# Kernel tuning notes

Measured on AMD Instinct MI355X. Metric: run time of the kernel, lower is better.

The kernel has to match this reference:

```python
import jax, jax.numpy as jnp
import numpy as np

IN_C = 256
OUT_C = 256
K = 3
PAD = 1
SCALE = 1.0 / np.sqrt(IN_C * K * K)  # 1/sqrt(in_channels * k^2)
EPS = 1e-8
NEG_SLOPE = 0.2


def setup_inputs() -> dict:
    key = jax.random.key(0)
    k0, k1, k2, k3 = jax.random.split(key, 4)
    B, H, W, SD = 8, 128, 128, 512
    x = jax.random.normal(k0, (B, IN_C, H, W), dtype=jnp.float32)
    style = jax.random.normal(k1, (B, SD), dtype=jnp.float32)
    weight = jax.random.normal(k2, (OUT_C, IN_C, K, K), dtype=jnp.float32)
    mod_w = jax.random.normal(k3, (IN_C, SD), dtype=jnp.float32) / np.sqrt(SD)
    mod_b = jnp.zeros((IN_C,), dtype=jnp.float32)
    return {"x": x, "style": style, "weight": weight, "mod_w": mod_w, "mod_b": mod_b}


def reference(x, style, weight, mod_w, mod_b):
    # modulation: Linear(style_dim -> in_channels)
    s = style @ mod_w.T + mod_b                      # [B, I]
    # per-sample modulated weight [B, O, I, k, k]
    w = SCALE * weight[None] * s[:, None, :, None, None]
    # demodulation over (I, kh, kw)
    demod = jax.lax.rsqrt(jnp.sum(w * w, axis=(2, 3, 4)) + EPS)  # [B, O]
    w = w * demod[:, :, None, None, None]
    # per-sample conv (equivalent to groups=batch trick), vmapped over batch
    def conv_one(xi, wi):  # xi: [I,H,W], wi: [O,I,k,k]
        return jax.lax.conv_general_dilated(
            xi[None], wi, window_strides=(1, 1),
            padding=((PAD, PAD), (PAD, PAD)),
            dimension_numbers=("NCHW", "OIHW", "NCHW"))[0]
    y = jax.vmap(conv_one)(x, w)                     # [B, O, H, W]
    # LeakyReLU(0.2)
    return jnp.where(y >= 0, y, NEG_SLOPE * y)
```

## Files before the change

### kernel.cpp

```cpp
#include <hip/hip_runtime.h>
#include <hip/hip_bf16.h>
#include <cstddef>
#include <cstdint>


#define IN_C 256
#define OUT_C 256
#define HW 16384
#define W_IMG 128
#define SDIM 512
#define SCALE_F 0.020833333333333332f
#define EPS_F 1e-8f
#define NEG_SLOPE 0.2f

#define XROWB 8320
#define WTILEB 8192

typedef short bf16x8 __attribute__((ext_vector_type(8)));
typedef float f32x4 __attribute__((ext_vector_type(4)));

__device__ __forceinline__ unsigned short f2bf(float f) {
  unsigned u = __builtin_bit_cast(unsigned, f);
  unsigned r = u + 0x7FFFu + ((u >> 16) & 1u);
  return (unsigned short)(r >> 16);
}

__device__ __forceinline__ void glds16(const void* g, void* l) {
  __builtin_amdgcn_global_load_lds(
      (const __attribute__((address_space(1))) unsigned int*)g,
      (__attribute__((address_space(3))) unsigned int*)l, 16, 0, 0);
}

__global__ void style_mod_kernel(const float* __restrict__ style,
                                 const float* __restrict__ mod_w,
                                 const float* __restrict__ mod_b,
                                 float* __restrict__ s_out) {
  const int b = blockIdx.x, iq = blockIdx.y;
  const int il = threadIdx.x >> 2, part = threadIdx.x & 3;
  const int i = iq * 64 + il;
  const float4* st4 = (const float4*)(style + (size_t)b * SDIM) + part * 32;
  const float4* mw4 = (const float4*)(mod_w + (size_t)i * SDIM) + part * 32;
  float a = 0.f;
#pragma unroll 8
  for (int j = 0; j < 32; ++j) {
    float4 s = st4[j], w = mw4[j];
    a += s.x * w.x + s.y * w.y + s.z * w.z + s.w * w.w;
  }
  a += __shfl_xor(a, 1);
  a += __shfl_xor(a, 2);
  if (part == 0) s_out[b * IN_C + i] = a + mod_b[i];
}

__global__ void wsq_kernel(const float* __restrict__ weight,
                           float* __restrict__ wsq) {
  const int o = blockIdx.x, i = threadIdx.x;
  const float* wp = weight + ((size_t)o * IN_C + i) * 9;
  float s = 0.f;
#pragma unroll
  for (int k = 0; k < 9; ++k) s += wp[k] * wp[k];
  wsq[o * IN_C + i] = s;
}

__global__ void demod_kernel(const float* __restrict__ wsq,
                             const float* __restrict__ s_in,
                             float* __restrict__ dscaled) {
  const int o = blockIdx.x, i = threadIdx.x;
  const float wq = wsq[o * IN_C + i];
  float vb[8];
#pragma unroll
  for (int b = 0; b < 8; ++b) {
    float sv = s_in[b * IN_C + i];
    vb[b] = sv * sv * wq;
  }
#pragma unroll
  for (int b = 0; b < 8; ++b)
#pragma unroll
    for (int off = 32; off > 0; off >>= 1) vb[b] += __shfl_down(vb[b], off);
  __shared__ float red[4][8];
  const int lane = threadIdx.x & 63, wvid = threadIdx.x >> 6;
  if (lane == 0) {
#pragma unroll
    for (int b = 0; b < 8; ++b) red[wvid][b] = vb[b];
  }
  __syncthreads();
  if (threadIdx.x < 8) {
    float t = red[0][threadIdx.x] + red[1][threadIdx.x] +
              red[2][threadIdx.x] + red[3][threadIdx.x];
    dscaled[threadIdx.x * OUT_C + o] = SCALE_F * rsqrtf(SCALE_F * SCALE_F * t + EPS_F);
  }
}

__global__ void wpack_kernel(const float* __restrict__ weight,
                             unsigned char* __restrict__ wbf) {
  int tap = blockIdx.x, oblk = blockIdx.y, iblk = blockIdx.z;
  unsigned char* dst = wbf + ((size_t)((tap * 2 + oblk) * 8 + iblk)) * WTILEB;
  for (int t = threadIdx.x; t < 512; t += 256) {
    int oo = t >> 2, c = t & 3;
    int cp = c ^ ((oo >> 1) & 3);
    int o = oblk * 128 + oo;
    bf16x8 v;
#pragma unroll
    for (int j = 0; j < 8; ++j) {
      int i = iblk * 32 + c * 8 + j;
      v[j] = (short)f2bf(weight[((size_t)o * IN_C + i) * 9 + tap]);
    }
    *(bf16x8*)(dst + oo * 64 + cp * 16) = v;
  }
}

__global__ void zfill_kernel(float4* __restrict__ zrow) {
  float4 z = {0.f, 0.f, 0.f, 0.f};
  for (int c = threadIdx.x; c < XROWB / 16; c += 256) zrow[c] = z;
}

__global__ __launch_bounds__(256) void xpack_kernel(
    const float* __restrict__ x, const float* __restrict__ s_in,
    unsigned char* __restrict__ xp) {
  __shared__ short xt[128 * 33];
  const int tid = threadIdx.x;
  const int rb = blockIdx.x, iblk = blockIdx.y, b = blockIdx.z;
  const float* xbase = x + ((size_t)(b * IN_C + iblk * 32)) * HW;
  const int chp = tid >> 5;
  const int lp = tid & 31;
  float sv[4];
#pragma unroll
  for (int p = 0; p < 4; ++p) sv[p] = s_in[b * IN_C + iblk * 32 + p * 8 + chp];

  for (int r = 0; r < 8; ++r) {
    const int row = rb * 8 + r;
#pragma unroll
    for (int p = 0; p < 4; ++p) {
      const int ch = p * 8 + chp;
      float4 v = *(const float4*)(xbase + (size_t)ch * HW + row * W_IMG + lp * 4);
      const int pix0 = lp * 4;
      xt[(pix0 + 0) * 33 + ch] = (short)f2bf(v.x * sv[p]);
      xt[(pix0 + 1) * 33 + ch] = (short)f2bf(v.y * sv[p]);
      xt[(pix0 + 2) * 33 + ch] = (short)f2bf(v.z * sv[p]);
      xt[(pix0 + 3) * 33 + ch] = (short)f2bf(v.w * sv[p]);
    }
    __syncthreads();
    unsigned char* dst = xp + ((size_t)((b * 8 + iblk) * 128 + row)) * XROWB;
    for (int task = tid; task < 520; task += 256) {
      int slot = task >> 2, c = task & 3;
      int cp = c ^ ((slot >> 1) & 3);
      int pix = slot - 1;
      bf16x8 v = (bf16x8)(short)0;
      if ((unsigned)pix < 128u) {
#pragma unroll
        for (int j = 0; j < 8; ++j) v[j] = xt[pix * 33 + c * 8 + j];
      }
      *(bf16x8*)(dst + slot * 64 + cp * 16) = v;
    }
    __syncthreads();
  }
}

__global__ __launch_bounds__(256, 2) void modconv_kernel(
    const unsigned char* __restrict__ xp, const unsigned char* __restrict__ wbf,
    const unsigned char* __restrict__ zrow, const float* __restrict__ dscaled,
    float* __restrict__ out) {
  __shared__ __align__(16) unsigned char lds[2 * XROWB + 3 * WTILEB];

  const int tid = threadIdx.x;
  const int lane = tid & 63;
  const int wv = tid >> 6;
  const int wr = wv >> 1;
  const int wc = wv & 1;
  const int oblk = blockIdx.x;
  const int hp = blockIdx.y;
  const int b = blockIdx.z;
  const int l15 = lane & 15, cc = lane >> 4;

  f32x4 acc[4][8] = {};

  const int axor = ((cc ^ ((l15 >> 1) & 3)) << 4);
  int aoff[4];
#pragma unroll
  for (int m = 0; m < 4; ++m)
    aoff[m] = 2 * XROWB + (wr * 64 + m * 16 + l15) * 64 + axor;

  const unsigned char* xpb = xp + ((size_t)(b * 8)) * 128 * XROWB;

  for (int i0 = 0; i0 < 8; ++i0) {
    for (int kh = 0; kh < 3; ++kh) {
      for (int task = wv; task < 41; task += 4) {
        if (task < 17) {
          int c = task * 64 + lane;
          if (task < 16 || lane < 16) {
            int q = (c >= 520) ? 1 : 0;
            int wdx = c - q * 520;
            int gr = 2 * hp + kh - 1 + q;
            const unsigned char* src =
                ((unsigned)gr < 128u)
                    ? xpb + ((size_t)(i0 * 128 + gr)) * XROWB + wdx * 16
                    : zrow + wdx * 16;
            glds16(src, lds + task * 1024);
          }
        } else {
          int t2 = task - 17;
          int c2 = t2 * 64 + lane;
          int kw = c2 >> 9, rest = c2 & 511;
          const unsigned char* src =
              wbf + ((size_t)(((kh * 3 + kw) * 2 + oblk) * 8 + i0)) * WTILEB +
              rest * 16;
          glds16(src, lds + 2 * XROWB + t2 * 1024);
        }
      }
      asm volatile("s_waitcnt vmcnt(0)" ::: "memory");
      __syncthreads();
#pragma unroll
      for (int kw = 0; kw < 3; ++kw) {
        bf16x8 a0 = *(const bf16x8*)(lds + kw * WTILEB + aoff[0]);
        bf16x8 a1 = *(const bf16x8*)(lds + kw * WTILEB + aoff[1]);
        bf16x8 a2 = *(const bf16x8*)(lds + kw * WTILEB + aoff[2]);
        bf16x8 a3 = *(const bf16x8*)(lds + kw * WTILEB + aoff[3]);
        __builtin_amdgcn_s_setprio(1);
#pragma unroll
        for (int n = 0; n < 8; ++n) {
          int slot = n * 16 + l15 + kw;
          bf16x8 bn = *(const bf16x8*)(lds + wc * XROWB + slot * 64 +
                                       ((cc ^ ((slot >> 1) & 3)) << 4));
          acc[0][n] = __builtin_amdgcn_mfma_f32_16x16x32_bf16(a0, bn, acc[0][n], 0, 0, 0);
          acc[1][n] = __builtin_amdgcn_mfma_f32_16x16x32_bf16(a1, bn, acc[1][n], 0, 0, 0);
          acc[2][n] = __builtin_amdgcn_mfma_f32_16x16x32_bf16(a2, bn, acc[2][n], 0, 0, 0);
          acc[3][n] = __builtin_amdgcn_mfma_f32_16x16x32_bf16(a3, bn, acc[3][n], 0, 0, 0);
        }
        __builtin_amdgcn_s_setprio(0);
      }
      __syncthreads();
    }
  }

  const float* db = dscaled + b * OUT_C + oblk * 128;
  const int r_out = 2 * hp + wc;
  float* ob = out + (((size_t)(b * OUT_C + oblk * 128)) << 14) + r_out * 128;
#pragma unroll
  for (int m = 0; m < 4; ++m) {
#pragma unroll
    for (int r = 0; r < 4; ++r) {
      int oo = wr * 64 + m * 16 + cc * 4 + r;
      float d = db[oo];
#pragma unroll
      for (int n = 0; n < 8; ++n) {
        float v = acc[m][n][r] * d;
        v = (v >= 0.f) ? v : NEG_SLOPE * v;
        ob[((size_t)oo << 14) + n * 16 + l15] = v;
      }
    }
  }
}

extern "C" void kernel_launch(void* const* d_in, const int* in_sizes, int n_in,
                              void* d_out, int out_size, void* d_ws,
                              size_t ws_size, hipStream_t stream) {
  const float* x = (const float*)d_in[0];
  const float* style = (const float*)d_in[1];
  const float* weight = (const float*)d_in[2];
  const float* mod_w = (const float*)d_in[3];
  const float* mod_b = (const float*)d_in[4];
  float* out = (float*)d_out;

  float* s_ws = (float*)d_ws;
  float* dsc = s_ws + 2048;
  float* wsq = dsc + 2048;
  unsigned char* wbf = (unsigned char*)(wsq + 65536);
  unsigned char* xp = wbf + (size_t)9 * 2 * 8 * WTILEB;
  unsigned char* zrow = xp + (size_t)8 * 8 * 128 * XROWB;

  style_mod_kernel<<<dim3(8, 4), dim3(256), 0, stream>>>(style, mod_w, mod_b, s_ws);
  wsq_kernel<<<dim3(256), dim3(256), 0, stream>>>(weight, wsq);
  demod_kernel<<<dim3(256), dim3(256), 0, stream>>>(wsq, s_ws, dsc);
  wpack_kernel<<<dim3(9, 2, 8), dim3(256), 0, stream>>>(weight, wbf);
  zfill_kernel<<<dim3(1), dim3(256), 0, stream>>>((float4*)zrow);
  xpack_kernel<<<dim3(16, 8, 8), dim3(256), 0, stream>>>(x, s_ws, xp);

  modconv_kernel<<<dim3(2, 64, 8), dim3(256), 0, stream>>>(xp, wbf, zrow, dsc, out);
}
```

Before: 432.6 us.

## Restructure modconv to one output row per block with double-buffered LDS and register weights

The conv kernel now computes one output row per block instead of two. Each iteration loads the weight A-fragments straight from global memory into registers rather than staging them in LDS, and double-buffers the single input row in LDS so the next row's load overlaps the current MFMAs. Blocks are remapped through a linear swizzled index so batches are interleaved across the grid. The small prep kernels are merged (wsq into demod, zfill into demod), and the weight-tile swizzle is removed because those tiles no longer pass through LDS. This trades LDS traffic and barriers for uncoalesced-ish global/L2 reads of the weights and halves the reuse of weights per block.

```diff
diff --git a/kernel.cpp b/kernel.cpp
--- a/kernel.cpp
+++ b/kernel.cpp
@@ -51,21 +51,19 @@
   if (part == 0) s_out[b * IN_C + i] = a + mod_b[i];
 }
 
-__global__ void wsq_kernel(const float* __restrict__ weight,
-                           float* __restrict__ wsq) {
+__global__ void demod_kernel(const float* __restrict__ weight,
+                             const float* __restrict__ s_in,
+                             float* __restrict__ dscaled,
+                             float4* __restrict__ zrow) {
   const int o = blockIdx.x, i = threadIdx.x;
+  if (o == 0) {
+    float4 z = {0.f, 0.f, 0.f, 0.f};
+    for (int c = i; c < XROWB / 16; c += 256) zrow[c] = z;
+  }
   const float* wp = weight + ((size_t)o * IN_C + i) * 9;
-  float s = 0.f;
-#pragma unroll
-  for (int k = 0; k < 9; ++k) s += wp[k] * wp[k];
-  wsq[o * IN_C + i] = s;
-}
-
-__global__ void demod_kernel(const float* __restrict__ wsq,
-                             const float* __restrict__ s_in,
-                             float* __restrict__ dscaled) {
-  const int o = blockIdx.x, i = threadIdx.x;
-  const float wq = wsq[o * IN_C + i];
+  float wq = 0.f;
+#pragma unroll
+  for (int k = 0; k < 9; ++k) wq += wp[k] * wp[k];
   float vb[8];
 #pragma unroll
   for (int b = 0; b < 8; ++b) {
@@ -86,7 +84,8 @@
   if (threadIdx.x < 8) {
     float t = red[0][threadIdx.x] + red[1][threadIdx.x] +
               red[2][threadIdx.x] + red[3][threadIdx.x];
-    dscaled[threadIdx.x * OUT_C + o] = SCALE_F * rsqrtf(SCALE_F * SCALE_F * t + EPS_F);
+    dscaled[threadIdx.x * OUT_C + o] =
+        SCALE_F * rsqrtf(SCALE_F * SCALE_F * t + EPS_F);
   }
 }
 
@@ -96,7 +95,6 @@
   unsigned char* dst = wbf + ((size_t)((tap * 2 + oblk) * 8 + iblk)) * WTILEB;
   for (int t = threadIdx.x; t < 512; t += 256) {
     int oo = t >> 2, c = t & 3;
-    int cp = c ^ ((oo >> 1) & 3);
     int o = oblk * 128 + oo;
     bf16x8 v;
 #pragma unroll
@@ -104,13 +102,8 @@
       int i = iblk * 32 + c * 8 + j;
       v[j] = (short)f2bf(weight[((size_t)o * IN_C + i) * 9 + tap]);
     }
-    *(bf16x8*)(dst + oo * 64 + cp * 16) = v;
-  }
-}
-
-__global__ void zfill_kernel(float4* __restrict__ zrow) {
-  float4 z = {0.f, 0.f, 0.f, 0.f};
-  for (int c = threadIdx.x; c < XROWB / 16; c += 256) zrow[c] = z;
+    *(bf16x8*)(dst + oo * 64 + c * 16) = v;
+  }
 }
 
 __global__ __launch_bounds__(256) void xpack_kernel(
@@ -159,81 +152,85 @@
     const unsigned char* __restrict__ xp, const unsigned char* __restrict__ wbf,
     const unsigned char* __restrict__ zrow, const float* __restrict__ dscaled,
     float* __restrict__ out) {
-  __shared__ __align__(16) unsigned char lds[2 * XROWB + 3 * WTILEB];
+  __shared__ __align__(16) unsigned char lds[2 * XROWB];
 
   const int tid = threadIdx.x;
   const int lane = tid & 63;
   const int wv = tid >> 6;
   const int wr = wv >> 1;
   const int wc = wv & 1;
-  const int oblk = blockIdx.x;
-  const int hp = blockIdx.y;
-  const int b = blockIdx.z;
   const int l15 = lane & 15, cc = lane >> 4;
 
-  f32x4 acc[4][8] = {};
-
-  const int axor = ((cc ^ ((l15 >> 1) & 3)) << 4);
-  int aoff[4];
-#pragma unroll
-  for (int m = 0; m < 4; ++m)
-    aoff[m] = 2 * XROWB + (wr * 64 + m * 16 + l15) * 64 + axor;
+  const int bid = blockIdx.x;
+  const int logical = (bid & 7) * 256 + (bid >> 3);
+  const int oblk = logical & 1;
+  const int h = (logical >> 1) & 127;
+  const int b = logical >> 8;
+
+  f32x4 acc[4][4] = {};
 
   const unsigned char* xpb = xp + ((size_t)(b * 8)) * 128 * XROWB;
-
-  for (int i0 = 0; i0 < 8; ++i0) {
-    for (int kh = 0; kh < 3; ++kh) {
-      for (int task = wv; task < 41; task += 4) {
-        if (task < 17) {
-          int c = task * 64 + lane;
-          if (task < 16 || lane < 16) {
-            int q = (c >= 520) ? 1 : 0;
-            int wdx = c - q * 520;
-            int gr = 2 * hp + kh - 1 + q;
-            const unsigned char* src =
-                ((unsigned)gr < 128u)
-                    ? xpb + ((size_t)(i0 * 128 + gr)) * XROWB + wdx * 16
-                    : zrow + wdx * 16;
-            glds16(src, lds + task * 1024);
-          }
-        } else {
-          int t2 = task - 17;
-          int c2 = t2 * 64 + lane;
-          int kw = c2 >> 9, rest = c2 & 511;
-          const unsigned char* src =
-              wbf + ((size_t)(((kh * 3 + kw) * 2 + oblk) * 8 + i0)) * WTILEB +
-              rest * 16;
-          glds16(src, lds + 2 * XROWB + t2 * 1024);
-        }
+  const int arow_off = (wr * 64 + l15) * 64 + cc * 16;
+
+  {
+    const unsigned char* src =
+        (h >= 1) ? xpb + ((size_t)(0 * 128 + (h - 1))) * XROWB : zrow;
+    for (int task = wv; task < 9; task += 4)
+      if (task < 8 || lane < 8)
+        glds16(src + task * 1024 + lane * 16, lds + task * 1024);
+  }
+  asm volatile("s_waitcnt vmcnt(0)" ::: "memory");
+  __syncthreads();
+
+  for (int t = 0; t < 24; ++t) {
+    const int kh = t >> 3, i0 = t & 7;
+    unsigned char* cbuf = lds + (t & 1) * XROWB;
+
+    bf16x8 a[3][4];
+#pragma unroll
+    for (int kw = 0; kw < 3; ++kw) {
+      const unsigned char* wt =
+          wbf + ((size_t)(((kh * 3 + kw) * 2 + oblk) * 8 + i0)) * WTILEB;
+#pragma unroll
+      for (int m = 0; m < 4; ++m)
+        a[kw][m] = *(const bf16x8*)(wt + m * 1024 + arow_off);
+    }
+
+    if (t < 23) {
+      const int nt = t + 1;
+      const int nkh = nt >> 3, ni0 = nt & 7;
+      const int gr = h + nkh - 1;
+      const unsigned char* src =
+          ((unsigned)gr < 128u) ? xpb + ((size_t)(ni0 * 128 + gr)) * XROWB
+                                : zrow;
+      unsigned char* nbuf = lds + (nt & 1) * XROWB;
+      for (int task = wv; task < 9; task += 4)
+        if (task < 8 || lane < 8)
+          glds16(src + task * 1024 + lane * 16, nbuf + task * 1024);
+    }
+
+#pragma unroll
+    for (int kw = 0; kw < 3; ++kw) {
+      __builtin_amdgcn_s_setprio(1);
+#pragma unroll
+      for (int n = 0; n < 4; ++n) {
+        const int slot = wc * 64 + n * 16 + l15 + kw;
+        bf16x8 bn = *(const bf16x8*)(cbuf + slot * 64 +
+                                     ((cc ^ ((slot >> 1) & 3)) << 4));
+        acc[0][n] = __builtin_amdgcn_mfma_f32_16x16x32_bf16(a[kw][0], bn, acc[0][n], 0, 0, 0);
+        acc[1][n] = __builtin_amdgcn_mfma_f32_16x16x32_bf16(a[kw][1], bn, acc[1][n], 0, 0, 0);
+        acc[2][n] = __builtin_amdgcn_mfma_f32_16x16x32_bf16(a[kw][2], bn, acc[2][n], 0, 0, 0);
+        acc[3][n] = __builtin_amdgcn_mfma_f32_16x16x32_bf16(a[kw][3], bn, acc[3][n], 0, 0, 0);
       }
-      asm volatile("s_waitcnt vmcnt(0)" ::: "memory");
-      __syncthreads();
-#pragma unroll
-      for (int kw = 0; kw < 3; ++kw) {
-        bf16x8 a0 = *(const bf16x8*)(lds + kw * WTILEB + aoff[0]);
-        bf16x8 a1 = *(const bf16x8*)(lds + kw * WTILEB + aoff[1]);
-        bf16x8 a2 = *(const bf16x8*)(lds + kw * WTILEB + aoff[2]);
-        bf16x8 a3 = *(const bf16x8*)(lds + kw * WTILEB + aoff[3]);
-        __builtin_amdgcn_s_setprio(1);
-#pragma unroll
-        for (int n = 0; n < 8; ++n) {
-          int slot = n * 16 + l15 + kw;
-          bf16x8 bn = *(const bf16x8*)(lds + wc * XROWB + slot * 64 +
-                                       ((cc ^ ((slot >> 1) & 3)) << 4));
-          acc[0][n] = __builtin_amdgcn_mfma_f32_16x16x32_bf16(a0, bn, acc[0][n], 0, 0, 0);
-          acc[1][n] = __builtin_amdgcn_mfma_f32_16x16x32_bf16(a1, bn, acc[1][n], 0, 0, 0);
-          acc[2][n] = __builtin_amdgcn_mfma_f32_16x16x32_bf16(a2, bn, acc[2][n], 0, 0, 0);
-          acc[3][n] = __builtin_amdgcn_mfma_f32_16x16x32_bf16(a3, bn, acc[3][n], 0, 0, 0);
-        }
-        __builtin_amdgcn_s_setprio(0);
-      }
-      __syncthreads();
-    }
+      __builtin_amdgcn_s_setprio(0);
+    }
+
+    asm volatile("s_waitcnt vmcnt(0)" ::: "memory");
+    __syncthreads();
   }
 
   const float* db = dscaled + b * OUT_C + oblk * 128;
-  const int r_out = 2 * hp + wc;
-  float* ob = out + (((size_t)(b * OUT_C + oblk * 128)) << 14) + r_out * 128;
+  float* ob = out + (((size_t)(b * OUT_C + oblk * 128)) << 14) + h * 128;
 #pragma unroll
   for (int m = 0; m < 4; ++m) {
 #pragma unroll
@@ -241,10 +238,10 @@
       int oo = wr * 64 + m * 16 + cc * 4 + r;
       float d = db[oo];
 #pragma unroll
-      for (int n = 0; n < 8; ++n) {
+      for (int n = 0; n < 4; ++n) {
         float v = acc[m][n][r] * d;
         v = (v >= 0.f) ? v : NEG_SLOPE * v;
-        ob[((size_t)oo << 14) + n * 16 + l15] = v;
+        ob[((size_t)oo << 14) + wc * 64 + n * 16 + l15] = v;
       }
     }
   }
@@ -262,17 +259,14 @@
 
   float* s_ws = (float*)d_ws;
   float* dsc = s_ws + 2048;
-  float* wsq = dsc + 2048;
-  unsigned char* wbf = (unsigned char*)(wsq + 65536);
+  unsigned char* wbf = (unsigned char*)(dsc + 2048);
   unsigned char* xp = wbf + (size_t)9 * 2 * 8 * WTILEB;
   unsigned char* zrow = xp + (size_t)8 * 8 * 128 * XROWB;
 
   style_mod_kernel<<<dim3(8, 4), dim3(256), 0, stream>>>(style, mod_w, mod_b, s_ws);
-  wsq_kernel<<<dim3(256), dim3(256), 0, stream>>>(weight, wsq);
-  demod_kernel<<<dim3(256), dim3(256), 0, stream>>>(wsq, s_ws, dsc);
+  demod_kernel<<<dim3(256), dim3(256), 0, stream>>>(weight, s_ws, dsc, (float4*)zrow);
   wpack_kernel<<<dim3(9, 2, 8), dim3(256), 0, stream>>>(weight, wbf);
-  zfill_kernel<<<dim3(1), dim3(256), 0, stream>>>((float4*)zrow);
   xpack_kernel<<<dim3(16, 8, 8), dim3(256), 0, stream>>>(x, s_ws, xp);
 
-  modconv_kernel<<<dim3(2, 64, 8), dim3(256), 0, stream>>>(xp, wbf, zrow, dsc, out);
-}
+  modconv_kernel<<<dim3(2048), dim3(256), 0, stream>>>(xp, wbf, zrow, dsc, out);
+}
```

Measured after the change: 416.9 us. 3.6% less time.
